# Optimization experiments

Measured on AMD Instinct MI355X. Metric: run time of the kernel, lower is better.

Reference implementation:

```python
import jax, jax.numpy as jnp
from jax import lax
import numpy as np

B, T, F, U = 256, 512, 32, 350


def setup_inputs() -> dict:
    key = jax.random.key(0)
    ks = jax.random.split(key, 5)
    # Glorot-normal-ish scales for weights
    kernel = jax.random.normal(ks[0], (F, 4 * U), jnp.float32) * np.sqrt(2.0 / (F + 4 * U))
    recurrent_kernel = jax.random.normal(ks[1], (U, 4 * U), jnp.float32) * np.sqrt(2.0 / (U + 4 * U))
    dense_w = jax.random.normal(ks[2], (U, 1), jnp.float32) * np.sqrt(2.0 / (U + 1))
    return {
        "x": jax.random.normal(ks[3], (B, T, F), jnp.float32),
        "kernel": kernel,
        "recurrent_kernel": recurrent_kernel,
        "bias": jnp.zeros((4 * U,), jnp.float32),
        "dense_w": dense_w,
        "dense_b": jnp.zeros((1,), jnp.float32),
    }


def reference(x, kernel, recurrent_kernel, bias, dense_w, dense_b):
    # Keras LSTM with activation='relu' (candidate + cell-output activation),
    # recurrent_activation=sigmoid (default). Gate order: i, f, c, o.
    b, t, f = x.shape
    u = recurrent_kernel.shape[0]
    # Precompute input projection for all timesteps: [B, T, 4U]
    xz = jnp.einsum('btf,fg->btg', x, kernel) + bias

    def step(carry, xt):
        h, c = carry
        z = xt + h @ recurrent_kernel  # [B, 4U]
        zi, zf, zg, zo = jnp.split(z, 4, axis=-1)
        i = jax.nn.sigmoid(zi)
        fg = jax.nn.sigmoid(zf)
        g = jax.nn.relu(zg)          # activation='relu' on candidate
        o = jax.nn.sigmoid(zo)
        c_new = fg * c + i * g
        h_new = o * jax.nn.relu(c_new)  # activation='relu' on output
        return (h_new, c_new), h_new

    h0 = jnp.zeros((b, u), x.dtype)
    c0 = jnp.zeros((b, u), x.dtype)
    (_, _), hs = lax.scan(step, (h0, c0), jnp.swapaxes(xz, 0, 1))  # hs: [T, B, U]
    hs = jnp.swapaxes(hs, 0, 1)  # [B, T, U] (return_sequences=True)
    return hs @ dense_w + dense_b  # [B, T, 1]
```

## Files before the change

### kernel.cpp

```cpp
#include <hip/hip_runtime.h>
#include <stdint.h>


#define T_   512
#define F_   32
#define U_   350
#define G4   1400
#define NGRP 16
#define NB   16
#define NCB  11
#define KC   12
#define NT   88
#define HSLOTUS 5632
#define SLOTW   5632

typedef __attribute__((ext_vector_type(8))) short  short8;
typedef __attribute__((ext_vector_type(4))) short  short4_;
typedef __attribute__((ext_vector_type(4))) float  float4_;
typedef unsigned long long u64t;

__device__ __forceinline__ short f2bf(float f) {
  union { float f; uint32_t u; } v; v.f = f;
  return (short)((v.u + 0x7FFFu + ((v.u >> 16) & 1u)) >> 16);
}

#define SZ_W     (NT*KC*64*8*2u)
#define OFF_XBF  (SZ_W)
#define SZ_XBF   (256u*T_*F_*2u)
#define OFF_HBUF (OFF_XBF + SZ_XBF)
#define SZ_HBUF  (NGRP*2u*HSLOTUS*2u)
#define OFF_HMIR (OFF_HBUF + SZ_HBUF)
#define SZ_HMIR  (NGRP*2u*SLOTW*4u)
#define OFF_TAG  (OFF_HMIR + SZ_HMIR)
#define SZ_TAG   (NGRP*2u*32u*4u)
#define OFF_FLG  (OFF_TAG + SZ_TAG)
#define SZ_FLG   (NGRP*16u*4u)
#define OFF_WP   (OFF_FLG + SZ_FLG)
#define SZ_WP    (NGRP*NCB*NB*T_*4u)

__global__ void prep_w(const float* __restrict__ kern,
                       const float* __restrict__ rk,
                       const float* __restrict__ bias,
                       short* __restrict__ wswz) {
  const int tile = blockIdx.x, lane = threadIdx.x;
  const int g = tile / 22, jt = tile % 22;
  const int colg = jt * 16 + (lane & 15);
  const int src = g * U_ + colg;
  const bool valid = (colg < U_);
  const int kbase = (lane >> 4) * 8;
  for (int kc = 0; kc < KC; ++kc) {
    short8 pack;
    #pragma unroll
    for (int jj = 0; jj < 8; ++jj) {
      int k = kc * 32 + kbase + jj;
      float v = 0.f;
      if (valid) {
        if (k < F_)            v = kern[k * G4 + src];
        else if (k < F_ + U_)  v = rk[(k - F_) * G4 + src];
        else if (k == F_ + U_) v = bias[src];
      }
      pack[jj] = f2bf(v);
    }
    *(short8*)(wswz + (((size_t)kc * NT + tile) * 64 + lane) * 8) = pack;
  }
}

__global__ void prep_x(const float* __restrict__ x, short* __restrict__ xbf) {
  int i = (blockIdx.x * 256 + threadIdx.x) * 4;
  float4_ v = *(const float4_*)(x + i);
  short4_ o;
  #pragma unroll
  for (int jj = 0; jj < 4; ++jj) o[jj] = f2bf(v[jj]);
  *(short4_*)(xbf + i) = o;
}

__global__ void init_all(unsigned short* __restrict__ hb16,
                         uint32_t* __restrict__ hmir32,
                         uint32_t* __restrict__ tagbuf,
                         uint32_t* __restrict__ flagbuf) {
  int i = blockIdx.x * 256 + threadIdx.x;
  int grp = i / HSLOTUS, rem = i % HSLOTUS;
  {
    int blk = rem >> 9, quadc = (rem >> 7) & 3, cpos = rem & 7;
    int col = blk * 32 + quadc * 8 + cpos;
    hb16[(size_t)(grp * 2 + 1) * HSLOTUS + rem] =
        (col == 350) ? (unsigned short)0x3F80 : 0;
  }
  {
    int blkm = rem >> 8, off = rem & 255;
    int fi = blkm >> 1, fk2 = blkm & 1, fquadc = off >> 6;
    int fk1 = (off >> 1) & 1, fb = off & 1;
    int fcol = fi * 32 + fquadc * 8 + fk2 * 4 + fk1 * 2 + fb;
    hmir32[(size_t)(grp * 2 + 1) * SLOTW + rem] =
        (fcol == 350) ? 0x3F800000u : 0u;
  }
  if (rem < 32) {
    tagbuf[(size_t)(grp * 2 + 0) * 32 + rem] = 0u;
    tagbuf[(size_t)(grp * 2 + 1) * 32 + rem] = 0u;
  }
  if (rem == 0) flagbuf[grp * 16] = 0u;
}

__global__ __launch_bounds__(128)
__attribute__((amdgpu_waves_per_eu(1, 1)))
void lstm_kernel(const short* __restrict__ xbf, const short* __restrict__ wswz,
                 unsigned short* __restrict__ hb16, uint32_t* __restrict__ hmir32,
                 uint32_t* __restrict__ tagbuf, uint32_t* __restrict__ flagbuf,
                 const float* __restrict__ dense_w, float* __restrict__ wpart) {
  __shared__ float lds_part[2][T_][16];

  const int tid  = threadIdx.x;
  const int lane = tid & 63;
  const int wv   = tid >> 6;
  const int l15  = lane & 15;
  const int quad = lane >> 4;
  const int grp  = blockIdx.x & 15;
  const int j    = blockIdx.x >> 4;
  const int tileg = 2 * j + wv;

  short8 wreg[4][KC];
  #pragma unroll
  for (int g = 0; g < 4; ++g)
    #pragma unroll
    for (int kc = 0; kc < KC; ++kc)
      wreg[g][kc] = *(const short8*)(wswz +
          (((size_t)kc * NT + (g * 22 + tileg)) * 64 + lane) * 8);

  const int col = tileg * 16 + l15;
  const float dwv = (col < U_) ? dense_w[col] : 0.f;
  float cst[4] = {0.f, 0.f, 0.f, 0.f};

  const int pblk = col >> 5, pc32 = col & 31;
  const int pbase_us = pblk * 512 + ((pc32 >> 3) * 16 + quad * 4) * 8 + (pc32 & 7);
  const int colrem = col & 31;
  const int fastoff = (((col >> 5) * 2 + ((colrem >> 2) & 1)) * 256)
                    + (((colrem >> 3) * 16 + quad * 4) * 4)
                    + (((colrem >> 1) & 1) * 2) + (col & 1);

  const short* xrow = xbf + ((size_t)(grp * NB + l15) * T_) * F_ + quad * 8;
  unsigned short* hbb = hb16 + (size_t)grp * 2 * HSLOTUS;
  uint32_t* hm  = hmir32 + (size_t)grp * 2 * SLOTW;
  uint32_t* tgg = tagbuf + (size_t)grp * 2 * 32;
  uint32_t* flagp = flagbuf + grp * 16;
  const int tagidx = (lane < 22) ? lane : 31;

  bool mm = false;
  const short hs_init = (col == 350) ? (short)0x3F80 : 0;
  uint32_t wout[4], wout_prev[4];
  #pragma unroll
  for (int r = 0; r < 4; ++r)
    wout[r] = wout_prev[r] = ((uint32_t)(unsigned short)hs_init) << 16;

  short8 axf = *(const short8*)(xrow);

  #pragma unroll 1
  for (int t = 0; t < T_; ++t) {
    const uint32_t want = (uint32_t)t;
    const uint32_t* tgr = tgg + (size_t)((t + 1) & 1) * 32;
    uint32_t tv = __hip_atomic_load(tgr + tagidx, __ATOMIC_RELAXED,
                                    __HIP_MEMORY_SCOPE_AGENT);

    float4_ acc[4];
    #pragma unroll
    for (int g = 0; g < 4; ++g) {
      float4_ z = (float4_){0.f, 0.f, 0.f, 0.f};
      acc[g] = __builtin_amdgcn_mfma_f32_16x16x32_bf16(axf, wreg[g][0], z, 0, 0, 0);
    }

    short8 afr[11];
    bool ready = (bool)__all((int)(lane >= 22 || tv == want));
    bool gotm = false;
    int tries = 0;
    while (!ready) {
      ++tries;
      if (!mm) {
        if ((tries & 63) == 0) {
          uint32_t f = __hip_atomic_load(flagp, __ATOMIC_RELAXED,
                                         __HIP_MEMORY_SCOPE_SYSTEM);
          if (f) mm = true;
        }
        if (tries == 16384) {
          if (lane == 0)
            __hip_atomic_store(flagp, 1u, __ATOMIC_RELAXED,
                               __HIP_MEMORY_SCOPE_SYSTEM);
          mm = true;
        }
        if (mm) {
          uint32_t* md1 = hm + (size_t)((t + 1) & 1) * SLOTW + fastoff;
          uint32_t* md0 = hm + (size_t)(t & 1) * SLOTW + fastoff;
          #pragma unroll
          for (int r = 0; r < 4; ++r) {
            __hip_atomic_store(md1 + r * 4, wout[r], __ATOMIC_RELAXED,
                               __HIP_MEMORY_SCOPE_AGENT);
            __hip_atomic_store(md0 + r * 4, wout_prev[r], __ATOMIC_RELAXED,
                               __HIP_MEMORY_SCOPE_AGENT);
          }
        }
      } else {
        const u64t* mq = (const u64t*)(hm + (size_t)((t + 1) & 1) * SLOTW)
                       + (size_t)lane * 2;
        u64t q[44];
        #pragma unroll
        for (int i = 0; i < 11; ++i) {
          const u64t* pa = mq + (size_t)(2 * i) * 128;
          const u64t* pb = mq + (size_t)(2 * i + 1) * 128;
          q[4 * i + 0] = __hip_atomic_load(pa,     __ATOMIC_RELAXED, __HIP_MEMORY_SCOPE_AGENT);
          q[4 * i + 1] = __hip_atomic_load(pa + 1, __ATOMIC_RELAXED, __HIP_MEMORY_SCOPE_AGENT);
          q[4 * i + 2] = __hip_atomic_load(pb,     __ATOMIC_RELAXED, __HIP_MEMORY_SCOPE_AGENT);
          q[4 * i + 3] = __hip_atomic_load(pb + 1, __ATOMIC_RELAXED, __HIP_MEMORY_SCOPE_AGENT);
        }
        const uint32_t tag16 = want & 0xFFFFu;
        uint32_t bad = 0;
        #pragma unroll
        for (int i = 0; i < 44; ++i) {
          bad |= ((uint32_t)q[i] ^ tag16);
          bad |= ((uint32_t)(q[i] >> 32) ^ tag16);
        }
        if ((bool)__all((int)((bad & 0xFFFFu) == 0))) {
          #pragma unroll
          for (int i = 0; i < 11; ++i) {
            union { uint32_t w[4]; short8 s; } u;
            #pragma unroll
            for (int k = 0; k < 4; ++k) {
              uint32_t lo = (uint32_t)q[4 * i + k];
              uint32_t hi = (uint32_t)(q[4 * i + k] >> 32);
              u.w[k] = (lo >> 16) | (hi & 0xFFFF0000u);
            }
            afr[i] = u.s;
          }
          gotm = true;
          break;
        }
      }
      tv = __hip_atomic_load(tgr + tagidx, __ATOMIC_RELAXED,
                             __HIP_MEMORY_SCOPE_AGENT);
      ready = (bool)__all((int)(lane >= 22 || tv == want));
    }

    if (!gotm) {
      const u64t* hq = (const u64t*)(hbb + (size_t)((t + 1) & 1) * HSLOTUS)
                     + (size_t)lane * 2;
      #pragma unroll
      for (int i = 0; i < 11; ++i) {
        union { u64t q[2]; short8 s; } u;
        u.q[0] = __hip_atomic_load(hq + (size_t)i * 128,     __ATOMIC_RELAXED, __HIP_MEMORY_SCOPE_AGENT);
        u.q[1] = __hip_atomic_load(hq + (size_t)i * 128 + 1, __ATOMIC_RELAXED, __HIP_MEMORY_SCOPE_AGENT);
        afr[i] = u.s;
      }
    }

    #pragma unroll
    for (int i = 0; i < 11; ++i)
      #pragma unroll
      for (int g = 0; g < 4; ++g)
        acc[g] = __builtin_amdgcn_mfma_f32_16x16x32_bf16(afr[i], wreg[g][i + 1], acc[g], 0, 0, 0);

    unsigned short* hwp = hbb + (size_t)(t & 1) * HSLOTUS + pbase_us;
    const uint32_t otag = (uint32_t)(t + 1);
    float hn[4];
    #pragma unroll
    for (int r = 0; r < 4; ++r) {
      float ig = __builtin_amdgcn_rcpf(1.f + __expf(-acc[0][r]));
      float fg = __builtin_amdgcn_rcpf(1.f + __expf(-acc[1][r]));
      float gg = fmaxf(acc[2][r], 0.f);
      float og = __builtin_amdgcn_rcpf(1.f + __expf(-acc[3][r]));
      float cn = fg * cst[r] + ig * gg;
      cst[r] = cn;
      hn[r] = og * fmaxf(cn, 0.f);
      short hs = f2bf(hn[r]);
      if (col == 350) hs = (short)0x3F80;
      else if (col == 351) hs = 0;
      wout_prev[r] = wout[r];
      wout[r] = (((uint32_t)(unsigned short)hs) << 16) | (otag & 0xFFFFu);
      hwp[r * 8] = (unsigned short)hs;
    }
    if (lane == 0)
      __hip_atomic_store(tgg + (size_t)(t & 1) * 32 + tileg, otag,
                         __ATOMIC_RELEASE, __HIP_MEMORY_SCOPE_WORKGROUP);

    short8 axf_nx;
    {
      const int tn = (t + 1 < T_) ? (t + 1) : 0;
      const u64t* xq = (const u64t*)(xrow + tn * F_);
      union { u64t q[2]; short8 s; } ux;
      ux.q[0] = __hip_atomic_load(xq,     __ATOMIC_RELAXED, __HIP_MEMORY_SCOPE_AGENT);
      ux.q[1] = __hip_atomic_load(xq + 1, __ATOMIC_RELAXED, __HIP_MEMORY_SCOPE_AGENT);
      axf_nx = ux.s;
    }

    if (mm) {
      uint32_t* hwrm = hm + (size_t)(t & 1) * SLOTW + fastoff;
      #pragma unroll
      for (int r = 0; r < 4; ++r)
        __hip_atomic_store(hwrm + r * 4, wout[r], __ATOMIC_RELAXED,
                           __HIP_MEMORY_SCOPE_AGENT);
    }

    #pragma unroll
    for (int r = 0; r < 4; ++r) {
      float s = hn[r] * dwv;
      s += __shfl_xor(s, 1); s += __shfl_xor(s, 2);
      s += __shfl_xor(s, 4); s += __shfl_xor(s, 8);
      if (l15 == 0) lds_part[wv][t][quad * 4 + r] = s;
    }

    axf = axf_nx;
  }

  __syncthreads();
  float* wp = wpart + ((size_t)(grp * NCB + j) * NB) * T_;
  for (int i = tid; i < NB * T_; i += 128) {
    int t = i & (T_ - 1), row = i >> 9;
    wp[(size_t)row * T_ + t] = lds_part[0][t][row] + lds_part[1][t][row];
  }
}

__global__ void reduce_out(const float* __restrict__ wpart,
                           const float* __restrict__ dense_b,
                           float* __restrict__ out) {
  int i = blockIdx.x * 256 + threadIdx.x;
  int b = i >> 9, t = i & 511;
  int grp = b >> 4, row = b & 15;
  float s = dense_b[0];
  #pragma unroll
  for (int j = 0; j < NCB; ++j)
    s += wpart[(((size_t)grp * NCB + j) * NB + row) * T_ + t];
  out[i] = s;
}

extern "C" void kernel_launch(void* const* d_in, const int* in_sizes, int n_in,
                              void* d_out, int out_size, void* d_ws, size_t ws_size,
                              hipStream_t stream) {
  const float* x    = (const float*)d_in[0];
  const float* kern = (const float*)d_in[1];
  const float* rk   = (const float*)d_in[2];
  const float* bias = (const float*)d_in[3];
  const float* dw   = (const float*)d_in[4];
  const float* db   = (const float*)d_in[5];
  float* out = (float*)d_out;

  char* ws = (char*)d_ws;
  short*          wswz   = (short*)(ws);
  short*          xbf    = (short*)(ws + OFF_XBF);
  unsigned short* hb16   = (unsigned short*)(ws + OFF_HBUF);
  uint32_t*       hmir32 = (uint32_t*)(ws + OFF_HMIR);
  uint32_t*       tagbuf = (uint32_t*)(ws + OFF_TAG);
  uint32_t*       flagbuf= (uint32_t*)(ws + OFF_FLG);
  float*          wpart  = (float*)(ws + OFF_WP);

  prep_w<<<NT, 64, 0, stream>>>(kern, rk, bias, wswz);
  prep_x<<<(256 * T_ * F_) / (256 * 4), 256, 0, stream>>>(x, xbf);
  init_all<<<(NGRP * HSLOTUS) / 256, 256, 0, stream>>>(hb16, hmir32, tagbuf, flagbuf);
  lstm_kernel<<<NGRP * NCB, 128, 0, stream>>>(xbf, wswz, hb16, hmir32, tagbuf,
                                              flagbuf, dw, wpart);
  reduce_out<<<(256 * T_) / 256, 256, 0, stream>>>(wpart, db, out);
}
```

Baseline: 948.0 us.

## Consume recurrent h chunks incrementally as producer tags arrive

The wait loop no longer blocks until all 11 K-chunks of the previous hidden state are ready. It ballots per-lane readiness tags, loads each 32-wide chunk whose producer tags are both set, and issues that chunk's MFMAs right away, tracking completion in a bitmask. The fallback mirror path is also made per-chunk, checking tags and accumulating one chunk at a time. This overlaps the recurrent matmul with waiting on slower producer blocks, at the cost of more divergent control flow and repeated tag polling.

```diff
diff --git a/kernel.cpp b/kernel.cpp
--- a/kernel.cpp
+++ b/kernel.cpp
@@ -157,8 +157,6 @@
   for (int t = 0; t < T_; ++t) {
     const uint32_t want = (uint32_t)t;
     const uint32_t* tgr = tgg + (size_t)((t + 1) & 1) * 32;
-    uint32_t tv = __hip_atomic_load(tgr + tagidx, __ATOMIC_RELAXED,
-                                    __HIP_MEMORY_SCOPE_AGENT);
 
     float4_ acc[4];
     #pragma unroll
@@ -167,13 +165,36 @@
       acc[g] = __builtin_amdgcn_mfma_f32_16x16x32_bf16(axf, wreg[g][0], z, 0, 0, 0);
     }
 
-    short8 afr[11];
-    bool ready = (bool)__all((int)(lane >= 22 || tv == want));
-    bool gotm = false;
+    const u64t* hq = (const u64t*)(hbb + (size_t)((t + 1) & 1) * HSLOTUS)
+                   + (size_t)lane * 2;
+    uint32_t done = 0;
     int tries = 0;
-    while (!ready) {
-      ++tries;
+    while (done != 0x7FFu) {
       if (!mm) {
+        uint32_t tv = __hip_atomic_load(tgr + tagidx, __ATOMIC_RELAXED,
+                                        __HIP_MEMORY_SCOPE_AGENT);
+        u64t rdy = __ballot((int)(lane >= 22 || tv == want));
+        uint32_t newm = 0;
+        short8 afr[11];
+        #pragma unroll
+        for (int i = 0; i < 11; ++i) {
+          if (!((done >> i) & 1u) && (((rdy >> (2 * i)) & 3ull) == 3ull)) {
+            union { u64t q[2]; short8 s; } u;
+            u.q[0] = __hip_atomic_load(hq + (size_t)i * 128,     __ATOMIC_RELAXED, __HIP_MEMORY_SCOPE_AGENT);
+            u.q[1] = __hip_atomic_load(hq + (size_t)i * 128 + 1, __ATOMIC_RELAXED, __HIP_MEMORY_SCOPE_AGENT);
+            afr[i] = u.s;
+            newm |= 1u << i;
+          }
+        }
+        #pragma unroll
+        for (int i = 0; i < 11; ++i)
+          if ((newm >> i) & 1u)
+            #pragma unroll
+            for (int g = 0; g < 4; ++g)
+              acc[g] = __builtin_amdgcn_mfma_f32_16x16x32_bf16(afr[i], wreg[g][i + 1], acc[g], 0, 0, 0);
+        done |= newm;
+        if (done == 0x7FFu) break;
+        ++tries;
         if ((tries & 63) == 0) {
           uint32_t f = __hip_atomic_load(flagp, __ATOMIC_RELAXED,
                                          __HIP_MEMORY_SCOPE_SYSTEM);
@@ -199,61 +220,33 @@
       } else {
         const u64t* mq = (const u64t*)(hm + (size_t)((t + 1) & 1) * SLOTW)
                        + (size_t)lane * 2;
-        u64t q[44];
+        const uint32_t tag16 = want & 0xFFFFu;
         #pragma unroll
         for (int i = 0; i < 11; ++i) {
-          const u64t* pa = mq + (size_t)(2 * i) * 128;
-          const u64t* pb = mq + (size_t)(2 * i + 1) * 128;
-          q[4 * i + 0] = __hip_atomic_load(pa,     __ATOMIC_RELAXED, __HIP_MEMORY_SCOPE_AGENT);
-          q[4 * i + 1] = __hip_atomic_load(pa + 1, __ATOMIC_RELAXED, __HIP_MEMORY_SCOPE_AGENT);
-          q[4 * i + 2] = __hip_atomic_load(pb,     __ATOMIC_RELAXED, __HIP_MEMORY_SCOPE_AGENT);
-          q[4 * i + 3] = __hip_atomic_load(pb + 1, __ATOMIC_RELAXED, __HIP_MEMORY_SCOPE_AGENT);
-        }
-        const uint32_t tag16 = want & 0xFFFFu;
-        uint32_t bad = 0;
-        #pragma unroll
-        for (int i = 0; i < 44; ++i) {
-          bad |= ((uint32_t)q[i] ^ tag16);
-          bad |= ((uint32_t)(q[i] >> 32) ^ tag16);
-        }
-        if ((bool)__all((int)((bad & 0xFFFFu) == 0))) {
-          #pragma unroll
-          for (int i = 0; i < 11; ++i) {
+          if ((done >> i) & 1u) continue;
+          u64t q0 = __hip_atomic_load(mq + (size_t)(2 * i) * 128,     __ATOMIC_RELAXED, __HIP_MEMORY_SCOPE_AGENT);
+          u64t q1 = __hip_atomic_load(mq + (size_t)(2 * i) * 128 + 1, __ATOMIC_RELAXED, __HIP_MEMORY_SCOPE_AGENT);
+          u64t q2 = __hip_atomic_load(mq + (size_t)(2 * i + 1) * 128,     __ATOMIC_RELAXED, __HIP_MEMORY_SCOPE_AGENT);
+          u64t q3 = __hip_atomic_load(mq + (size_t)(2 * i + 1) * 128 + 1, __ATOMIC_RELAXED, __HIP_MEMORY_SCOPE_AGENT);
+          uint32_t bad = 0;
+          bad |= ((uint32_t)q0 ^ tag16) | ((uint32_t)(q0 >> 32) ^ tag16);
+          bad |= ((uint32_t)q1 ^ tag16) | ((uint32_t)(q1 >> 32) ^ tag16);
+          bad |= ((uint32_t)q2 ^ tag16) | ((uint32_t)(q2 >> 32) ^ tag16);
+          bad |= ((uint32_t)q3 ^ tag16) | ((uint32_t)(q3 >> 32) ^ tag16);
+          if ((bool)__all((int)((bad & 0xFFFFu) == 0))) {
             union { uint32_t w[4]; short8 s; } u;
+            u.w[0] = ((uint32_t)q0 >> 16) | ((uint32_t)(q0 >> 32) & 0xFFFF0000u);
+            u.w[1] = ((uint32_t)q1 >> 16) | ((uint32_t)(q1 >> 32) & 0xFFFF0000u);
+            u.w[2] = ((uint32_t)q2 >> 16) | ((uint32_t)(q2 >> 32) & 0xFFFF0000u);
+            u.w[3] = ((uint32_t)q3 >> 16) | ((uint32_t)(q3 >> 32) & 0xFFFF0000u);
             #pragma unroll
-            for (int k = 0; k < 4; ++k) {
-              uint32_t lo = (uint32_t)q[4 * i + k];
-              uint32_t hi = (uint32_t)(q[4 * i + k] >> 32);
-              u.w[k] = (lo >> 16) | (hi & 0xFFFF0000u);
-            }
-            afr[i] = u.s;
+            for (int g = 0; g < 4; ++g)
+              acc[g] = __builtin_amdgcn_mfma_f32_16x16x32_bf16(u.s, wreg[g][i + 1], acc[g], 0, 0, 0);
+            done |= 1u << i;
           }
-          gotm = true;
-          break;
         }
       }
-      tv = __hip_atomic_load(tgr + tagidx, __ATOMIC_RELAXED,
-                             __HIP_MEMORY_SCOPE_AGENT);
-      ready = (bool)__all((int)(lane >= 22 || tv == want));
-    }
-
-    if (!gotm) {
-      const u64t* hq = (const u64t*)(hbb + (size_t)((t + 1) & 1) * HSLOTUS)
-                     + (size_t)lane * 2;
-      #pragma unroll
-      for (int i = 0; i < 11; ++i) {
-        union { u64t q[2]; short8 s; } u;
-        u.q[0] = __hip_atomic_load(hq + (size_t)i * 128,     __ATOMIC_RELAXED, __HIP_MEMORY_SCOPE_AGENT);
-        u.q[1] = __hip_atomic_load(hq + (size_t)i * 128 + 1, __ATOMIC_RELAXED, __HIP_MEMORY_SCOPE_AGENT);
-        afr[i] = u.s;
-      }
-    }
-
-    #pragma unroll
-    for (int i = 0; i < 11; ++i)
-      #pragma unroll
-      for (int g = 0; g < 4; ++g)
-        acc[g] = __builtin_amdgcn_mfma_f32_16x16x32_bf16(afr[i], wreg[g][i + 1], acc[g], 0, 0, 0);
+    }
 
     unsigned short* hwp = hbb + (size_t)(t & 1) * HSLOTUS + pbase_us;
     const uint32_t otag = (uint32_t)(t + 1);
```

Result: slower. 1.622 ms (+71.1%).
